# Kernel tuning notes

Hardware: AMD Instinct MI355X
Metric: run time of the kernel (lower is better)

The kernel has to match this reference:

```python
import jax, jax.numpy as jnp
import numpy as np

D = 1024
EXPAND = 2
DI = EXPAND * D
K = 4           # d_conv
C = 64          # chunk_size
ALPHA = 0.9     # memory decay
B, S = 2, 8192
EPS = 1e-5


def setup_inputs() -> dict:
    key = jax.random.key(0)
    ks = jax.random.split(key, 10)
    s = 0.02
    return {
        "x": jax.random.normal(ks[0], (B, S, D), dtype=jnp.float32),
        "norm_w": jnp.ones((D,), dtype=jnp.float32),
        "w_up": jax.random.normal(ks[1], (D, DI), dtype=jnp.float32) * s,
        "w_gate": jax.random.normal(ks[2], (D, DI), dtype=jnp.float32) * s,
        "w_down": jax.random.normal(ks[3], (DI, D), dtype=jnp.float32) * s,
        "conv_w": jax.random.normal(ks[4], (K, 1, DI), dtype=jnp.float32) * s,  # WIO depthwise
        "conv_b": jnp.zeros((DI,), dtype=jnp.float32),
        "wq": jax.random.normal(ks[5], (D, D), dtype=jnp.float32) * s,
        "wk": jax.random.normal(ks[6], (D, D), dtype=jnp.float32) * s,
        "wv": jax.random.normal(ks[7], (D, D), dtype=jnp.float32) * s,
        "wo": jax.random.normal(ks[8], (D, D), dtype=jnp.float32) * s,
    }


def _rmsnorm(x, w):
    ms = jnp.mean(jnp.square(x.astype(jnp.float32)), axis=-1, keepdims=True)
    return (x * jax.lax.rsqrt(ms + EPS).astype(x.dtype)) * w


def _causal_depthwise_conv(u, conv_w, conv_b):
    # u: [B,S,DI]; depthwise causal conv over S, then SiLU
    y = jax.lax.conv_general_dilated(
        u, conv_w,
        window_strides=(1,), padding=[(K - 1, 0)],
        dimension_numbers=("NWC", "WIO", "NWC"),
        feature_group_count=DI)
    return jax.nn.silu(y + conv_b)


def _hebbian_memory(h, wq, wk, wv, wo):
    # chunked linear-attention style Hebbian memory
    b, s, d = h.shape
    n = s // C
    scale = d ** -0.5
    q = (h @ wq).reshape(b, n, C, d) * scale
    k = (h @ wk).reshape(b, n, C, d)
    v = (h @ wv).reshape(b, n, C, d)
    mask = jnp.tril(jnp.ones((C, C), dtype=h.dtype))  # inclusive causal within chunk

    def step(M, qkv):
        qc, kc, vc = qkv  # [b,C,d]
        inter = jnp.einsum("bcd,bde->bce", qc, M)
        attn = jnp.einsum("bcd,bed->bce", qc, kc) * mask
        intra = jnp.einsum("bce,bed->bcd", attn, vc)
        M_new = ALPHA * M + jnp.einsum("bcd,bce->bde", kc, vc)
        return M_new, inter + intra

    M0 = jnp.zeros((b, d, d), dtype=h.dtype)
    qkv = (jnp.swapaxes(q, 0, 1), jnp.swapaxes(k, 0, 1), jnp.swapaxes(v, 0, 1))
    _, o = jax.lax.scan(step, M0, qkv)        # [n,b,C,d]
    o = jnp.swapaxes(o, 0, 1).reshape(b, s, d)
    return o @ wo


def reference(x, norm_w, w_up, w_gate, w_down, conv_w, conv_b, wq, wk, wv, wo):
    normed = _rmsnorm(x, norm_w)
    val = _causal_depthwise_conv(normed @ w_up, conv_w, conv_b)   # [B,S,DI]
    gate = jax.nn.silu(normed @ w_gate)
    out = (gate * val) @ w_down                                   # [B,S,D]
    out = _hebbian_memory(out, wq, wk, wv, wo)
    return x + out
```

## Files before the change

### kernel.cpp

```cpp
#include <hip/hip_runtime.h>
#include <cstdint>
#include <cstddef>

#define SS 8192
#define DD 1024
#define DI2 2048
#define NR 16384

#define LOG2_09 (-0.152003093445050f)
#define LAMBDA16 0.185302018885184f

typedef __attribute__((ext_vector_type(4))) float f32x4;
typedef __attribute__((ext_vector_type(8))) __bf16 bf16x8;

union U16 { uint4 u; bf16x8 b; };

static __device__ __forceinline__ f32x4 MFMA(uint4 a, uint4 b, f32x4 c) {
  U16 ua, ub; ua.u = a; ub.u = b;
  return __builtin_amdgcn_mfma_f32_16x16x32_bf16(ua.b, ub.b, c, 0, 0, 0);
}

static __device__ __forceinline__ unsigned short f2bf(float f) {
  union { float f; unsigned u; } v; v.f = f;
  return (unsigned short)((v.u + 0x7FFFu + ((v.u >> 16) & 1u)) >> 16);
}
static __device__ __forceinline__ float bf2f(unsigned b) {
  union { unsigned u; float f; } v; v.u = b << 16; return v.f;
}
static __device__ __forceinline__ void unpack8(uint4 u, float* f) {
  f[0] = bf2f(u.x & 0xFFFFu); f[1] = bf2f(u.x >> 16);
  f[2] = bf2f(u.y & 0xFFFFu); f[3] = bf2f(u.y >> 16);
  f[4] = bf2f(u.z & 0xFFFFu); f[5] = bf2f(u.z >> 16);
  f[6] = bf2f(u.w & 0xFFFFu); f[7] = bf2f(u.w >> 16);
}

static __device__ __forceinline__ void glds16(const unsigned short* g, char* l) {
  __builtin_amdgcn_global_load_lds(
      (const __attribute__((address_space(1))) unsigned int*)g,
      (__attribute__((address_space(3))) unsigned int*)l, 16, 0, 0);
}

__global__ __launch_bounds__(256)
void transpose_cast(const float* __restrict__ in, unsigned short* __restrict__ out, int R, int Cc) {
  __shared__ float tile[32][33];
  const int r0 = blockIdx.y * 32, c0 = blockIdx.x * 32;
  const int tx = threadIdx.x, ty = threadIdx.y;
#pragma unroll
  for (int i = 0; i < 4; i++)
    tile[ty + i * 8][tx] = in[(size_t)(r0 + ty + i * 8) * Cc + c0 + tx];
  __syncthreads();
#pragma unroll
  for (int i = 0; i < 4; i++)
    out[(size_t)(c0 + ty + i * 8) * R + r0 + tx] = f2bf(tile[tx][ty + i * 8]);
}

__global__ __launch_bounds__(256)
void rmsnorm_kernel(const float* __restrict__ x, const float* __restrict__ w,
                    unsigned short* __restrict__ out) {
  const int row = blockIdx.x, t = threadIdx.x;
  const float4 v = ((const float4*)(x + (size_t)row * DD))[t];
  float ss = v.x * v.x + v.y * v.y + v.z * v.z + v.w * v.w;
  __shared__ float sred[256];
  sred[t] = ss;
  __syncthreads();
  for (int o = 128; o > 0; o >>= 1) {
    if (t < o) sred[t] += sred[t + o];
    __syncthreads();
  }
  const float rr = rsqrtf(sred[0] * (1.0f / (float)DD) + 1e-5f);
  const float4 wv = ((const float4*)w)[t];
  uint2 pk;
  pk.x = (unsigned)f2bf(v.x * rr * wv.x) | ((unsigned)f2bf(v.y * rr * wv.y) << 16);
  pk.y = (unsigned)f2bf(v.z * rr * wv.z) | ((unsigned)f2bf(v.w * rr * wv.w) << 16);
  *(uint2*)(out + (size_t)row * DD + t * 4) = pk;
}

enum { EP_BF16 = 0, EP_BF16_BOTH = 1, EP_BF16_T = 2, EP_F32_RES = 3, EP_STATE = 4,
       EP_SCORE = 6, EP_PVX = 7, EP_QKV = 8 };

template <int MODE>
__global__ __launch_bounds__(512, 2)
void gemm256(const unsigned short* __restrict__ A, const unsigned short* __restrict__ Bt,
             unsigned short* __restrict__ Cb, unsigned short* __restrict__ Ct,
             float* __restrict__ Cf, const float* __restrict__ resid,
             unsigned short* __restrict__ Cx,
             int M, int N, int kLen, int lda, int ldb, float scale) {
  __shared__ char sLds[131072];
  const int t = threadIdx.x, lane = t & 63, wid = t >> 6;
  const int wr = wid >> 2, wc = wid & 3;
  const int l15 = lane & 15, lh = lane >> 4;
  const int mblocks = M >> 8;
  int m0, n0;
  if constexpr (MODE == EP_SCORE) {
    const int p = (int)blockIdx.x;
    const int mt = (p >= 6) ? 3 : (p >= 3) ? 2 : (p >= 1) ? 1 : 0;
    const int nt = p - ((mt * (mt + 1)) >> 1);
    m0 = mt << 8; n0 = nt << 8;
  } else if ((mblocks & 7) == 0) {
    const int msl = mblocks >> 3;
    const int xcd = (int)blockIdx.x & 7, loc = (int)blockIdx.x >> 3;
    m0 = (xcd * msl + (loc % msl)) << 8;
    n0 = (loc / msl) << 8;
  } else {
    m0 = ((int)blockIdx.x % mblocks) << 8;
    n0 = ((int)blockIdx.x / mblocks) << 8;
  }
  int zb = 0, zg = 0;
  const unsigned short* Abase = A;
  const unsigned short* Bbase = Bt;
  if constexpr (MODE == EP_STATE || MODE == EP_SCORE || MODE == EP_PVX) {
    const int gb = blockIdx.z;
    zb = gb >> 3; zg = gb & 7;
    if constexpr (MODE == EP_STATE) {
      Abase = A + (size_t)zb * DD * SS + (size_t)zg * 1024;
      Bbase = Bt + (size_t)zb * DD * SS + (size_t)zg * 1024;
    } else if constexpr (MODE == EP_SCORE) {
      Abase = A + ((size_t)zb * SS + (size_t)zg * 1024) * (size_t)lda;
      Bbase = Bt + ((size_t)zb * SS + (size_t)zg * 1024) * (size_t)ldb;
    } else {
      Abase = A + ((size_t)blockIdx.z << 20);
      Bbase = Bt + (size_t)zb * DD * SS + (size_t)zg * 1024;
    }
  }
  const int srow = wid * 16 + (lane >> 2);
  const int scol = ((lane & 3) << 3) ^ (((srow >> 1) & 3) << 3);
  const unsigned short* pA0 = Abase + (size_t)(m0 + srow) * lda + scol;
  const unsigned short* pA1 = pA0 + (size_t)128 * lda;
  const unsigned short* pB0 = Bbase + (size_t)(n0 + srow) * ldb + scol;
  const unsigned short* pB1 = pB0 + (size_t)128 * ldb;
  const int ldsW = wid * 1024;
  int ntV = 0;
  const unsigned short *pA2 = nullptr, *pA2h = nullptr, *pB2 = nullptr, *pB2h = nullptr;
  if constexpr (MODE == EP_PVX) {
    ntV = ((m0 >> 8) + 1) << 3;
    const unsigned short* qsb = Cx + ((size_t)zb * SS + (size_t)zg * 1024) * DD;
    pA2  = qsb + (size_t)(m0 + srow) * DD + scol;
    pA2h = pA2 + (size_t)128 * DD;
    const unsigned short* mnb = Ct + ((size_t)blockIdx.z << 20);
    pB2  = mnb + (size_t)(n0 + srow) * 1024 + scol;
    pB2h = pB2 + (size_t)128 * 1024;
  }
  int offA[8], offB[4];
#pragma unroll
  for (int mf = 0; mf < 8; mf++) {
    const int r = wr * 128 + mf * 16 + l15;
    offA[mf] = r * 64 + ((lh * 16) ^ (((r >> 1) & 3) << 4));
  }
#pragma unroll
  for (int nf = 0; nf < 4; nf++) {
    const int r = wc * 64 + nf * 16 + l15;
    offB[nf] = r * 64 + ((lh * 16) ^ (((r >> 1) & 3) << 4));
  }
  int NT = kLen >> 5;
  if constexpr (MODE == EP_PVX) NT = ntV + 32;
#define BUFA(tt) (sLds + ((tt) & 3) * 32768)
#define BUFB(tt) (sLds + ((tt) & 3) * 32768 + 16384)
  auto stage = [&](int tt) {
    const int _k = tt * 32;
    const unsigned short* a0 = pA0 + _k;
    const unsigned short* a1 = pA1 + _k;
    const unsigned short* b0 = pB0 + _k;
    const unsigned short* b1 = pB1 + _k;
    if constexpr (MODE == EP_PVX) {
      if (tt >= ntV) {
        const int k2 = (tt - ntV) * 32;
        a0 = pA2 + k2; a1 = pA2h + k2;
        b0 = pB2 + k2; b1 = pB2h + k2;
      }
    }
    glds16(a0, BUFA(tt) + ldsW);
    glds16(a1, BUFA(tt) + 8192 + ldsW);
    glds16(b0, BUFB(tt) + ldsW);
    glds16(b1, BUFB(tt) + 8192 + ldsW);
  };
  stage(0); stage(1); stage(2);
  asm volatile("s_waitcnt vmcnt(8)" ::: "memory");
  __builtin_amdgcn_s_barrier();
  f32x4 acc[8][4] = {};
  for (int kt = 0; kt < NT; ++kt) {
    const char* At  = BUFA(kt);
    const char* Bt_ = BUFB(kt);
    uint4 av[8], bv[4];
#pragma unroll
    for (int i = 0; i < 8; i++) av[i] = *(const uint4*)(At + offA[i]);
#pragma unroll
    for (int i = 0; i < 4; i++) bv[i] = *(const uint4*)(Bt_ + offB[i]);
    if (kt + 3 < NT) stage(kt + 3);
    __builtin_amdgcn_s_setprio(1);
#pragma unroll
    for (int mf = 0; mf < 8; mf++)
#pragma unroll
      for (int nf = 0; nf < 4; nf++)
        acc[mf][nf] = MFMA(av[mf], bv[nf], acc[mf][nf]);
    __builtin_amdgcn_s_setprio(0);
    if (kt < NT - 3)       { asm volatile("s_waitcnt vmcnt(8)" ::: "memory"); }
    else if (kt == NT - 3) { asm volatile("s_waitcnt vmcnt(4)" ::: "memory"); }
    else if (kt == NT - 2) { asm volatile("s_waitcnt vmcnt(0)" ::: "memory"); }
    __builtin_amdgcn_s_barrier();
  }
#undef BUFA
#undef BUFB
#pragma unroll
  for (int mf = 0; mf < 8; mf++) {
    const int r0 = m0 + wr * 128 + mf * 16 + lh * 4;
#pragma unroll
    for (int nf = 0; nf < 4; nf++) {
      const int c = n0 + wc * 64 + nf * 16 + l15;
      f32x4 v = acc[mf][nf] * scale;
      if constexpr (MODE == EP_F32_RES) {
#pragma unroll
        for (int jj = 0; jj < 4; jj++) {
          const size_t idx = (size_t)(r0 + jj) * N + c;
          Cf[idx] = v[jj] + resid[idx];
        }
      } else if constexpr (MODE == EP_STATE) {
        unsigned short* Tg = Cb + ((size_t)blockIdx.z << 20);
#pragma unroll
        for (int jj = 0; jj < 4; jj++)
          Tg[(size_t)(r0 + jj) * 1024 + c] = f2bf(v[jj]);
      } else if constexpr (MODE == EP_SCORE) {
        unsigned short* Sg = Cb + ((size_t)blockIdx.z << 20);
        const int qt = r0 >> 6;
        const int tb = c >> 6;
        float w;
        if (tb > qt)       w = 0.0f;
        else if (tb == qt) w = 1.0f;
        else               w = exp2f((float)(qt - 1 - tb) * LOG2_09);
#pragma unroll
        for (int jj = 0; jj < 4; jj++) {
          float val = v[jj] * w;
          if (tb == qt && (c & 63) > ((r0 + jj) & 63)) val = 0.0f;
          Sg[(size_t)(r0 + jj) * 1024 + c] = f2bf(val);
        }
      } else if constexpr (MODE == EP_PVX) {
#pragma unroll
        for (int jj = 0; jj < 4; jj++)
          Cb[((size_t)zb * SS + (size_t)zg * 1024 + r0 + jj) * DD + c] = f2bf(v[jj]);
      } else if constexpr (MODE == EP_QKV) {
        unsigned short* qb  = Cb;
        unsigned short* kb  = Ct;
        unsigned short* ktb = (unsigned short*)Cf;
        unsigned short* vtb = (unsigned short*)const_cast<float*>(resid);
        const int sect = c >> 10, cc = c & 1023;
        const int bb = r0 >> 13, s0 = r0 & (SS - 1);
        if (sect == 0) {
          const float wq_row = exp2f((float)((s0 >> 6) & 15) * LOG2_09);
#pragma unroll
          for (int jj = 0; jj < 4; jj++) {
            qb[(size_t)(r0 + jj) * DD + cc] = f2bf(v[jj] * 0.03125f);
            Cx[(size_t)(r0 + jj) * DD + cc] = f2bf(v[jj] * 0.03125f * wq_row);
          }
        } else if (sect == 1) {
#pragma unroll
          for (int jj = 0; jj < 4; jj++)
            kb[(size_t)(r0 + jj) * DD + cc] = f2bf(v[jj]);
          const float wt = exp2f((float)(15 - ((s0 >> 6) & 15)) * LOG2_09);
          uint2 pk;
          pk.x = (unsigned)f2bf(v[0] * wt) | ((unsigned)f2bf(v[1] * wt) << 16);
          pk.y = (unsigned)f2bf(v[2] * wt) | ((unsigned)f2bf(v[3] * wt) << 16);
          *(uint2*)(ktb + ((size_t)bb * DD + cc) * SS + s0) = pk;
        } else {
          uint2 pk;
          pk.x = (unsigned)f2bf(v[0]) | ((unsigned)f2bf(v[1]) << 16);
          pk.y = (unsigned)f2bf(v[2]) | ((unsigned)f2bf(v[3]) << 16);
          *(uint2*)(vtb + ((size_t)bb * DD + cc) * SS + s0) = pk;
        }
      } else {
        if constexpr (MODE == EP_BF16 || MODE == EP_BF16_BOTH) {
#pragma unroll
          for (int jj = 0; jj < 4; jj++)
            Cb[(size_t)(r0 + jj) * N + c] = f2bf(v[jj]);
        }
        if constexpr (MODE == EP_BF16_BOTH || MODE == EP_BF16_T) {
          const int bb = r0 >> 13, s0 = r0 & (SS - 1);
          float wt = 1.0f;
          if constexpr (MODE == EP_BF16_BOTH)
            wt = exp2f((float)(15 - ((s0 >> 6) & 15)) * LOG2_09);
          uint2 pk;
          pk.x = (unsigned)f2bf(v[0] * wt) | ((unsigned)f2bf(v[1] * wt) << 16);
          pk.y = (unsigned)f2bf(v[2] * wt) | ((unsigned)f2bf(v[3] * wt) << 16);
          *(uint2*)(Ct + ((size_t)bb * DD + c) * SS + s0) = pk;
        }
      }
    }
  }
}

__global__ __launch_bounds__(256)
void convgate_kernel(const unsigned short* __restrict__ ug, const float* __restrict__ cw,
                     const float* __restrict__ cb, unsigned short* __restrict__ hin) {
  const int r = blockIdx.x;
  const int c0 = threadIdx.x * 8;
  const int s = r & (SS - 1);
  float acc[8];
#pragma unroll
  for (int i = 0; i < 8; i++) acc[i] = cb[c0 + i];
  for (int tap = 0; tap < 4; tap++) {
    const int ds = s - 3 + tap;
    if (ds < 0) continue;
    uint4 uv = *(const uint4*)(ug + (size_t)(r - 3 + tap) * 4096 + c0);
    float u[8]; unpack8(uv, u);
#pragma unroll
    for (int i = 0; i < 8; i++) acc[i] += u[i] * cw[tap * DI2 + c0 + i];
  }
  uint4 gv = *(const uint4*)(ug + (size_t)r * 4096 + DI2 + c0);
  float gt[8]; unpack8(gv, gt);
  unsigned short o16[8];
#pragma unroll
  for (int i = 0; i < 8; i++) {
    const float val = acc[i] / (1.0f + __expf(-acc[i]));
    const float gg  = gt[i] / (1.0f + __expf(-gt[i]));
    o16[i] = f2bf(val * gg);
  }
  uint4 ov;
  ov.x = (unsigned)o16[0] | ((unsigned)o16[1] << 16);
  ov.y = (unsigned)o16[2] | ((unsigned)o16[3] << 16);
  ov.z = (unsigned)o16[4] | ((unsigned)o16[5] << 16);
  ov.w = (unsigned)o16[6] | ((unsigned)o16[7] << 16);
  *(uint4*)(hin + (size_t)r * DI2 + c0) = ov;
}

__global__ __launch_bounds__(256)
void prefix_kernel(unsigned short* __restrict__ Tb) {
  const int tid = blockIdx.x * 256 + threadIdx.x;
  const int b = tid >> 17, i = tid & 131071;
  unsigned short* p = Tb + (((size_t)b * 8) << 20) + (size_t)i * 8;
  float acc[8] = {};
  for (int g = 0; g < 8; g++) {
    unsigned short* pg = p + ((size_t)g << 20);
    uint4 tv = *(uint4*)pg;
    float tf_[8]; unpack8(tv, tf_);
    uint4 ov;
    ov.x = (unsigned)f2bf(acc[0]) | ((unsigned)f2bf(acc[1]) << 16);
    ov.y = (unsigned)f2bf(acc[2]) | ((unsigned)f2bf(acc[3]) << 16);
    ov.z = (unsigned)f2bf(acc[4]) | ((unsigned)f2bf(acc[5]) << 16);
    ov.w = (unsigned)f2bf(acc[6]) | ((unsigned)f2bf(acc[7]) << 16);
    *(uint4*)pg = ov;
#pragma unroll
    for (int e = 0; e < 8; e++) acc[e] = LAMBDA16 * acc[e] + tf_[e];
  }
}

extern "C" void kernel_launch(void* const* d_in, const int* in_sizes, int n_in,
                              void* d_out, int out_size, void* d_ws, size_t ws_size,
                              hipStream_t stream) {
  (void)in_sizes; (void)n_in; (void)out_size;
  const float* x      = (const float*)d_in[0];
  const float* norm_w = (const float*)d_in[1];
  const float* w_up   = (const float*)d_in[2];
  const float* w_gate = (const float*)d_in[3];
  const float* w_down = (const float*)d_in[4];
  const float* conv_w = (const float*)d_in[5];
  const float* conv_b = (const float*)d_in[6];
  const float* wq     = (const float*)d_in[7];
  const float* wk     = (const float*)d_in[8];
  const float* wv     = (const float*)d_in[9];
  const float* wo     = (const float*)d_in[10];
  float* out = (float*)d_out;

  const size_t MB = 1ull << 20;
  if (ws_size < 212 * MB) return;
  char* base = (char*)d_ws;
  unsigned short* ug     = (unsigned short*)(base + 0);
  unsigned short* hbuf   = (unsigned short*)(base + 0);
  unsigned short* Tbuf   = (unsigned short*)(base + 0);
  unsigned short* qbuf   = (unsigned short*)(base + 32 * MB);
  unsigned short* kbuf   = (unsigned short*)(base + 64 * MB);
  unsigned short* obuf   = (unsigned short*)(base + 64 * MB);
  unsigned short* ktbuf  = (unsigned short*)(base + 96 * MB);
  unsigned short* sbuf   = (unsigned short*)(base + 96 * MB);
  unsigned short* normed = (unsigned short*)(base + 128 * MB);
  unsigned short* hin    = (unsigned short*)(base + 128 * MB);
  unsigned short* vtbuf  = (unsigned short*)(base + 128 * MB);
  unsigned short* qsbuf  = (unsigned short*)(base + 160 * MB);
  unsigned short* wugt   = (unsigned short*)(base + 192 * MB);
  unsigned short* wdt    = (unsigned short*)(base + 200 * MB);
  unsigned short* wqkvt  = (unsigned short*)(base + 204 * MB);
  unsigned short* wot    = (unsigned short*)(base + 210 * MB);

  dim3 tb(32, 8);
  transpose_cast<<<dim3(DI2 / 32, DD / 32), tb, 0, stream>>>(w_up,   wugt,                    DD,  DI2);
  transpose_cast<<<dim3(DI2 / 32, DD / 32), tb, 0, stream>>>(w_gate, wugt + (size_t)DI2 * DD, DD,  DI2);
  transpose_cast<<<dim3(DD / 32, DI2 / 32), tb, 0, stream>>>(w_down, wdt, DI2, DD);
  transpose_cast<<<dim3(DD / 32, DD / 32),  tb, 0, stream>>>(wq, wqkvt,                          DD, DD);
  transpose_cast<<<dim3(DD / 32, DD / 32),  tb, 0, stream>>>(wk, wqkvt + (size_t)DD * DD,       DD, DD);
  transpose_cast<<<dim3(DD / 32, DD / 32),  tb, 0, stream>>>(wv, wqkvt + (size_t)2 * DD * DD,   DD, DD);
  transpose_cast<<<dim3(DD / 32, DD / 32),  tb, 0, stream>>>(wo, wot, DD, DD);

  rmsnorm_kernel<<<NR, 256, 0, stream>>>(x, norm_w, normed);

  gemm256<EP_BF16><<<dim3((NR / 256) * (4096 / 256)), 512, 0, stream>>>(
      normed, wugt, ug, nullptr, nullptr, nullptr, nullptr, NR, 4096, DD, DD, DD, 1.0f);

  convgate_kernel<<<NR, 256, 0, stream>>>(ug, conv_w, conv_b, hin);

  gemm256<EP_BF16><<<dim3((NR / 256) * (DD / 256)), 512, 0, stream>>>(
      hin, wdt, hbuf, nullptr, nullptr, nullptr, nullptr, NR, DD, DI2, DI2, DI2, 1.0f);

  gemm256<EP_QKV><<<dim3((NR / 256) * (3072 / 256)), 512, 0, stream>>>(
      hbuf, wqkvt, qbuf, kbuf, (float*)ktbuf, (const float*)vtbuf, qsbuf,
      NR, 3072, DD, DD, DD, 1.0f);

  gemm256<EP_STATE><<<dim3(16, 1, 16), 512, 0, stream>>>(
      vtbuf, ktbuf, Tbuf, nullptr, nullptr, nullptr, nullptr,
      1024, 1024, 1024, SS, SS, 1.0f);
  gemm256<EP_SCORE><<<dim3(10, 1, 16), 512, 0, stream>>>(
      qbuf, kbuf, sbuf, nullptr, nullptr, nullptr, nullptr,
      1024, 1024, 1024, DD, DD, 1.0f);
  prefix_kernel<<<1024, 256, 0, stream>>>(Tbuf);
  gemm256<EP_PVX><<<dim3(16, 1, 16), 512, 0, stream>>>(
      sbuf, vtbuf, obuf, Tbuf, nullptr, nullptr, qsbuf,
      1024, 1024, 1024, 1024, SS, 1.0f);

  gemm256<EP_F32_RES><<<dim3((NR / 256) * (DD / 256)), 512, 0, stream>>>(
      obuf, wot, nullptr, nullptr, out, x, nullptr, NR, DD, DD, DD, DD, 1.0f);
}
```

Measured before the change: 644.3 us.

## Add 8-phase ping-pong GEMM kernel for the dense projection GEMMs

Result: slower. 683.6 us (+6.1%).

```diff
diff --git a/kernel.cpp b/kernel.cpp
--- a/kernel.cpp
+++ b/kernel.cpp
@@ -77,6 +77,200 @@
 
 enum { EP_BF16 = 0, EP_BF16_BOTH = 1, EP_BF16_T = 2, EP_F32_RES = 3, EP_STATE = 4,
        EP_SCORE = 6, EP_PVX = 7, EP_QKV = 8 };
+
+template <int MODE>
+static __device__ __forceinline__ void dense_epilogue(
+    f32x4 (&acc)[8][4], int m0, int n0, int wr, int wc, int l15, int lh,
+    unsigned short* Cb, unsigned short* Ct, float* Cf, const float* resid,
+    unsigned short* Cx, int N, float scale) {
+#pragma unroll
+  for (int mf = 0; mf < 8; mf++) {
+    const int r0 = m0 + wr * 128 + mf * 16 + lh * 4;
+#pragma unroll
+    for (int nf = 0; nf < 4; nf++) {
+      const int c = n0 + wc * 64 + nf * 16 + l15;
+      f32x4 v = acc[mf][nf] * scale;
+      if constexpr (MODE == EP_F32_RES) {
+#pragma unroll
+        for (int jj = 0; jj < 4; jj++) {
+          const size_t idx = (size_t)(r0 + jj) * N + c;
+          Cf[idx] = v[jj] + resid[idx];
+        }
+      } else if constexpr (MODE == EP_QKV) {
+        unsigned short* qb  = Cb;
+        unsigned short* kb  = Ct;
+        unsigned short* ktb = (unsigned short*)Cf;
+        unsigned short* vtb = (unsigned short*)const_cast<float*>(resid);
+        const int sect = c >> 10, cc = c & 1023;
+        const int bb = r0 >> 13, s0 = r0 & (SS - 1);
+        if (sect == 0) {
+          const float wq_row = exp2f((float)((s0 >> 6) & 15) * LOG2_09);
+#pragma unroll
+          for (int jj = 0; jj < 4; jj++) {
+            qb[(size_t)(r0 + jj) * DD + cc] = f2bf(v[jj] * 0.03125f);
+            Cx[(size_t)(r0 + jj) * DD + cc] = f2bf(v[jj] * 0.03125f * wq_row);
+          }
+        } else if (sect == 1) {
+#pragma unroll
+          for (int jj = 0; jj < 4; jj++)
+            kb[(size_t)(r0 + jj) * DD + cc] = f2bf(v[jj]);
+          const float wt = exp2f((float)(15 - ((s0 >> 6) & 15)) * LOG2_09);
+          uint2 pk;
+          pk.x = (unsigned)f2bf(v[0] * wt) | ((unsigned)f2bf(v[1] * wt) << 16);
+          pk.y = (unsigned)f2bf(v[2] * wt) | ((unsigned)f2bf(v[3] * wt) << 16);
+          *(uint2*)(ktb + ((size_t)bb * DD + cc) * SS + s0) = pk;
+        } else {
+          uint2 pk;
+          pk.x = (unsigned)f2bf(v[0]) | ((unsigned)f2bf(v[1]) << 16);
+          pk.y = (unsigned)f2bf(v[2]) | ((unsigned)f2bf(v[3]) << 16);
+          *(uint2*)(vtb + ((size_t)bb * DD + cc) * SS + s0) = pk;
+        }
+      } else {
+#pragma unroll
+        for (int jj = 0; jj < 4; jj++)
+          Cb[(size_t)(r0 + jj) * N + c] = f2bf(v[jj]);
+      }
+    }
+  }
+}
+
+template <int MODE>
+__global__ __launch_bounds__(512, 2)
+void gemm8p(const unsigned short* __restrict__ A, const unsigned short* __restrict__ Bt,
+            unsigned short* __restrict__ Cb, unsigned short* __restrict__ Ct,
+            float* __restrict__ Cf, const float* __restrict__ resid,
+            unsigned short* __restrict__ Cx,
+            int M, int N, int kLen, int lda, int ldb, float scale) {
+  __shared__ char sLds[131072];
+  const int t = threadIdx.x, lane = t & 63, wid = t >> 6;
+  const int wr = wid >> 2, wc = wid & 3;
+  const int l15 = lane & 15, lh = lane >> 4;
+  const int mblocks = M >> 8;
+  int m0, n0;
+  if ((mblocks & 7) == 0) {
+    const int msl = mblocks >> 3;
+    const int xcd = (int)blockIdx.x & 7, loc = (int)blockIdx.x >> 3;
+    m0 = (xcd * msl + (loc % msl)) << 8;
+    n0 = (loc / msl) << 8;
+  } else {
+    m0 = ((int)blockIdx.x % mblocks) << 8;
+    n0 = ((int)blockIdx.x / mblocks) << 8;
+  }
+  const int rA = wid * 16 + (lane >> 3);
+  const int scol = (((lane & 7) ^ ((lane >> 3) & 7))) * 8;
+  const int NT = kLen >> 6;
+  int offA[2][8], offB[2][4];
+#pragma unroll
+  for (int qm = 0; qm < 2; qm++)
+#pragma unroll
+    for (int mfl = 0; mfl < 4; mfl++)
+#pragma unroll
+      for (int kk = 0; kk < 2; kk++) {
+        const int Rl = qm * 64 + mfl * 16 + l15;
+        offA[qm][mfl * 2 + kk] = wr * 16384 + Rl * 128 +
+                                 ((kk * 64 + lh * 16) ^ ((Rl & 7) << 4));
+      }
+#pragma unroll
+  for (int qn = 0; qn < 2; qn++)
+#pragma unroll
+    for (int nfl = 0; nfl < 2; nfl++)
+#pragma unroll
+      for (int kk = 0; kk < 2; kk++) {
+        const int Rl = (wc & 1) * 64 + (qn * 2 + nfl) * 16 + l15;
+        offB[qn][nfl * 2 + kk] = 65536 + (wc >> 1) * 16384 + Rl * 128 +
+                                 ((kk * 64 + lh * 16) ^ ((Rl & 7) << 4));
+      }
+  auto stageA = [&](int tile, int h) {
+    const unsigned short* src = A + (size_t)(m0 + h * 128 + rA) * lda + (size_t)tile * 64 + scol;
+    char* slot = sLds + (((tile & 1) * 2 + h) * 16384) + wid * 2048;
+    glds16(src, slot);
+    glds16(src + (size_t)8 * lda, slot + 1024);
+  };
+  auto stageB = [&](int tile, int h) {
+    const unsigned short* src = Bt + (size_t)(n0 + h * 128 + rA) * ldb + (size_t)tile * 64 + scol;
+    char* slot = sLds + 65536 + (((tile & 1) * 2 + h) * 16384) + wid * 2048;
+    glds16(src, slot);
+    glds16(src + (size_t)8 * ldb, slot + 1024);
+  };
+  stageB(0, 0); stageB(0, 1); stageA(0, 0); stageA(0, 1);
+  if (NT > 1) { stageB(1, 0); stageB(1, 1); }
+  asm volatile("s_waitcnt vmcnt(4)" ::: "memory");
+  __builtin_amdgcn_s_barrier();
+  f32x4 acc[8][4] = {};
+  uint4 av0[8], av1[8], bv0[4], bv1[4];
+  for (int kt = 0; kt < NT; ++kt) {
+    const int pb = (kt & 1) * 32768;
+    const char* L = sLds + pb;
+#pragma unroll
+    for (int i = 0; i < 8; i++) av0[i] = *(const uint4*)(L + offA[0][i]);
+#pragma unroll
+    for (int i = 0; i < 4; i++) bv0[i] = *(const uint4*)(L + offB[0][i]);
+    if (kt + 1 < NT) stageA(kt + 1, 0);
+    __builtin_amdgcn_s_barrier();
+    asm volatile("s_waitcnt lgkmcnt(0)" ::: "memory");
+    __builtin_amdgcn_sched_barrier(0);
+    __builtin_amdgcn_s_setprio(1);
+#pragma unroll
+    for (int mf = 0; mf < 4; mf++)
+#pragma unroll
+      for (int nf = 0; nf < 2; nf++)
+#pragma unroll
+        for (int kk = 0; kk < 2; kk++)
+          acc[mf][nf] = MFMA(av0[mf * 2 + kk], bv0[nf * 2 + kk], acc[mf][nf]);
+    __builtin_amdgcn_s_setprio(0);
+    __builtin_amdgcn_s_barrier();
+#pragma unroll
+    for (int i = 0; i < 4; i++) bv1[i] = *(const uint4*)(L + offB[1][i]);
+    if (kt + 1 < NT) stageA(kt + 1, 1);
+    __builtin_amdgcn_s_barrier();
+    asm volatile("s_waitcnt lgkmcnt(0)" ::: "memory");
+    __builtin_amdgcn_sched_barrier(0);
+    __builtin_amdgcn_s_setprio(1);
+#pragma unroll
+    for (int mf = 0; mf < 4; mf++)
+#pragma unroll
+      for (int nf = 0; nf < 2; nf++)
+#pragma unroll
+        for (int kk = 0; kk < 2; kk++)
+          acc[mf][2 + nf] = MFMA(av0[mf * 2 + kk], bv1[nf * 2 + kk], acc[mf][2 + nf]);
+    __builtin_amdgcn_s_setprio(0);
+    __builtin_amdgcn_s_barrier();
+#pragma unroll
+    for (int i = 0; i < 8; i++) av1[i] = *(const uint4*)(L + offA[1][i]);
+    if (kt + 2 < NT) stageB(kt + 2, 0);
+    __builtin_amdgcn_s_barrier();
+    asm volatile("s_waitcnt lgkmcnt(0)" ::: "memory");
+    __builtin_amdgcn_sched_barrier(0);
+    __builtin_amdgcn_s_setprio(1);
+#pragma unroll
+    for (int mf = 0; mf < 4; mf++)
+#pragma unroll
+      for (int nf = 0; nf < 2; nf++)
+#pragma unroll
+        for (int kk = 0; kk < 2; kk++)
+          acc[4 + mf][2 + nf] = MFMA(av1[mf * 2 + kk], bv1[nf * 2 + kk], acc[4 + mf][2 + nf]);
+    __builtin_amdgcn_s_setprio(0);
+    __builtin_amdgcn_s_barrier();
+    if (kt + 2 < NT) {
+      stageB(kt + 2, 1);
+      asm volatile("s_waitcnt vmcnt(4)" ::: "memory");
+    } else if (kt + 1 < NT) {
+      asm volatile("s_waitcnt vmcnt(0)" ::: "memory");
+    }
+    __builtin_amdgcn_s_barrier();
+    __builtin_amdgcn_s_setprio(1);
+#pragma unroll
+    for (int mf = 0; mf < 4; mf++)
+#pragma unroll
+      for (int nf = 0; nf < 2; nf++)
+#pragma unroll
+        for (int kk = 0; kk < 2; kk++)
+          acc[4 + mf][nf] = MFMA(av1[mf * 2 + kk], bv0[nf * 2 + kk], acc[4 + mf][nf]);
+    __builtin_amdgcn_s_setprio(0);
+    __builtin_amdgcn_s_barrier();
+  }
+  dense_epilogue<MODE>(acc, m0, n0, wr, wc, l15, lh, Cb, Ct, Cf, resid, Cx, N, scale);
+}
 
 template <int MODE>
 __global__ __launch_bounds__(512, 2)
@@ -96,11 +290,6 @@
     const int mt = (p >= 6) ? 3 : (p >= 3) ? 2 : (p >= 1) ? 1 : 0;
     const int nt = p - ((mt * (mt + 1)) >> 1);
     m0 = mt << 8; n0 = nt << 8;
-  } else if ((mblocks & 7) == 0) {
-    const int msl = mblocks >> 3;
-    const int xcd = (int)blockIdx.x & 7, loc = (int)blockIdx.x >> 3;
-    m0 = (xcd * msl + (loc % msl)) << 8;
-    n0 = (loc / msl) << 8;
   } else {
     m0 = ((int)blockIdx.x % mblocks) << 8;
     n0 = ((int)blockIdx.x / mblocks) << 8;
@@ -108,7 +297,7 @@
   int zb = 0, zg = 0;
   const unsigned short* Abase = A;
   const unsigned short* Bbase = Bt;
-  if constexpr (MODE == EP_STATE || MODE == EP_SCORE || MODE == EP_PVX) {
+  {
     const int gb = blockIdx.z;
     zb = gb >> 3; zg = gb & 7;
     if constexpr (MODE == EP_STATE) {
@@ -207,13 +396,7 @@
     for (int nf = 0; nf < 4; nf++) {
       const int c = n0 + wc * 64 + nf * 16 + l15;
       f32x4 v = acc[mf][nf] * scale;
-      if constexpr (MODE == EP_F32_RES) {
-#pragma unroll
-        for (int jj = 0; jj < 4; jj++) {
-          const size_t idx = (size_t)(r0 + jj) * N + c;
-          Cf[idx] = v[jj] + resid[idx];
-        }
-      } else if constexpr (MODE == EP_STATE) {
+      if constexpr (MODE == EP_STATE) {
         unsigned short* Tg = Cb + ((size_t)blockIdx.z << 20);
 #pragma unroll
         for (int jj = 0; jj < 4; jj++)
@@ -236,51 +419,6 @@
 #pragma unroll
         for (int jj = 0; jj < 4; jj++)
           Cb[((size_t)zb * SS + (size_t)zg * 1024 + r0 + jj) * DD + c] = f2bf(v[jj]);
-      } else if constexpr (MODE == EP_QKV) {
-        unsigned short* qb  = Cb;
-        unsigned short* kb  = Ct;
-        unsigned short* ktb = (unsigned short*)Cf;
-        unsigned short* vtb = (unsigned short*)const_cast<float*>(resid);
-        const int sect = c >> 10, cc = c & 1023;
-        const int bb = r0 >> 13, s0 = r0 & (SS - 1);
-        if (sect == 0) {
-          const float wq_row = exp2f((float)((s0 >> 6) & 15) * LOG2_09);
-#pragma unroll
-          for (int jj = 0; jj < 4; jj++) {
-            qb[(size_t)(r0 + jj) * DD + cc] = f2bf(v[jj] * 0.03125f);
-            Cx[(size_t)(r0 + jj) * DD + cc] = f2bf(v[jj] * 0.03125f * wq_row);
-          }
-        } else if (sect == 1) {
-#pragma unroll
-          for (int jj = 0; jj < 4; jj++)
-            kb[(size_t)(r0 + jj) * DD + cc] = f2bf(v[jj]);
-          const float wt = exp2f((float)(15 - ((s0 >> 6) & 15)) * LOG2_09);
-          uint2 pk;
-          pk.x = (unsigned)f2bf(v[0] * wt) | ((unsigned)f2bf(v[1] * wt) << 16);
-          pk.y = (unsigned)f2bf(v[2] * wt) | ((unsigned)f2bf(v[3] * wt) << 16);
-          *(uint2*)(ktb + ((size_t)bb * DD + cc) * SS + s0) = pk;
-        } else {
-          uint2 pk;
-          pk.x = (unsigned)f2bf(v[0]) | ((unsigned)f2bf(v[1]) << 16);
-          pk.y = (unsigned)f2bf(v[2]) | ((unsigned)f2bf(v[3]) << 16);
-          *(uint2*)(vtb + ((size_t)bb * DD + cc) * SS + s0) = pk;
-        }
-      } else {
-        if constexpr (MODE == EP_BF16 || MODE == EP_BF16_BOTH) {
-#pragma unroll
-          for (int jj = 0; jj < 4; jj++)
-            Cb[(size_t)(r0 + jj) * N + c] = f2bf(v[jj]);
-        }
-        if constexpr (MODE == EP_BF16_BOTH || MODE == EP_BF16_T) {
-          const int bb = r0 >> 13, s0 = r0 & (SS - 1);
-          float wt = 1.0f;
-          if constexpr (MODE == EP_BF16_BOTH)
-            wt = exp2f((float)(15 - ((s0 >> 6) & 15)) * LOG2_09);
-          uint2 pk;
-          pk.x = (unsigned)f2bf(v[0] * wt) | ((unsigned)f2bf(v[1] * wt) << 16);
-          pk.y = (unsigned)f2bf(v[2] * wt) | ((unsigned)f2bf(v[3] * wt) << 16);
-          *(uint2*)(Ct + ((size_t)bb * DD + c) * SS + s0) = pk;
-        }
       }
     }
   }
@@ -389,15 +527,15 @@
 
   rmsnorm_kernel<<<NR, 256, 0, stream>>>(x, norm_w, normed);
 
-  gemm256<EP_BF16><<<dim3((NR / 256) * (4096 / 256)), 512, 0, stream>>>(
+  gemm8p<EP_BF16><<<dim3((NR / 256) * (4096 / 256)), 512, 0, stream>>>(
       normed, wugt, ug, nullptr, nullptr, nullptr, nullptr, NR, 4096, DD, DD, DD, 1.0f);
 
   convgate_kernel<<<NR, 256, 0, stream>>>(ug, conv_w, conv_b, hin);
 
-  gemm256<EP_BF16><<<dim3((NR / 256) * (DD / 256)), 512, 0, stream>>>(
+  gemm8p<EP_BF16><<<dim3((NR / 256) * (DD / 256)), 512, 0, stream>>>(
       hin, wdt, hbuf, nullptr, nullptr, nullptr, nullptr, NR, DD, DI2, DI2, DI2, 1.0f);
 
-  gemm256<EP_QKV><<<dim3((NR / 256) * (3072 / 256)), 512, 0, stream>>>(
+  gemm8p<EP_QKV><<<dim3((NR / 256) * (3072 / 256)), 512, 0, stream>>>(
       hbuf, wqkvt, qbuf, kbuf, (float*)ktbuf, (const float*)vtbuf, qsbuf,
       NR, 3072, DD, DD, DD, 1.0f);
 
@@ -412,6 +550,6 @@
       sbuf, vtbuf, obuf, Tbuf, nullptr, nullptr, qsbuf,
       1024, 1024, 1024, 1024, SS, 1.0f);
 
-  gemm256<EP_F32_RES><<<dim3((NR / 256) * (DD / 256)), 512, 0, stream>>>(
+  gemm8p<EP_F32_RES><<<dim3((NR / 256) * (DD / 256)), 512, 0, stream>>>(
       obuf, wot, nullptr, nullptr, out, x, nullptr, NR, DD, DD, DD, DD, 1.0f);
 }
```

## Fuse state and score GEMMs into one launch and drop duplicate scaled-q buffer

Applied to the files above, without the earlier changes.

Result: no change. 648.3 us (+0.6%).

```diff
diff --git a/kernel.cpp b/kernel.cpp
--- a/kernel.cpp
+++ b/kernel.cpp
@@ -75,8 +75,7 @@
   *(uint2*)(out + (size_t)row * DD + t * 4) = pk;
 }
 
-enum { EP_BF16 = 0, EP_BF16_BOTH = 1, EP_BF16_T = 2, EP_F32_RES = 3, EP_STATE = 4,
-       EP_SCORE = 6, EP_PVX = 7, EP_QKV = 8 };
+enum { EP_BF16 = 0, EP_F32_RES = 3, EP_PVX = 7, EP_QKV = 8 };
 
 template <int MODE>
 __global__ __launch_bounds__(512, 2)
@@ -91,12 +90,7 @@
   const int l15 = lane & 15, lh = lane >> 4;
   const int mblocks = M >> 8;
   int m0, n0;
-  if constexpr (MODE == EP_SCORE) {
-    const int p = (int)blockIdx.x;
-    const int mt = (p >= 6) ? 3 : (p >= 3) ? 2 : (p >= 1) ? 1 : 0;
-    const int nt = p - ((mt * (mt + 1)) >> 1);
-    m0 = mt << 8; n0 = nt << 8;
-  } else if ((mblocks & 7) == 0) {
+  if ((mblocks & 7) == 0) {
     const int msl = mblocks >> 3;
     const int xcd = (int)blockIdx.x & 7, loc = (int)blockIdx.x >> 3;
     m0 = (xcd * msl + (loc % msl)) << 8;
@@ -108,19 +102,11 @@
   int zb = 0, zg = 0;
   const unsigned short* Abase = A;
   const unsigned short* Bbase = Bt;
-  if constexpr (MODE == EP_STATE || MODE == EP_SCORE || MODE == EP_PVX) {
+  if constexpr (MODE == EP_PVX) {
     const int gb = blockIdx.z;
     zb = gb >> 3; zg = gb & 7;
-    if constexpr (MODE == EP_STATE) {
-      Abase = A + (size_t)zb * DD * SS + (size_t)zg * 1024;
-      Bbase = Bt + (size_t)zb * DD * SS + (size_t)zg * 1024;
-    } else if constexpr (MODE == EP_SCORE) {
-      Abase = A + ((size_t)zb * SS + (size_t)zg * 1024) * (size_t)lda;
-      Bbase = Bt + ((size_t)zb * SS + (size_t)zg * 1024) * (size_t)ldb;
-    } else {
-      Abase = A + ((size_t)blockIdx.z << 20);
-      Bbase = Bt + (size_t)zb * DD * SS + (size_t)zg * 1024;
-    }
+    Abase = A + ((size_t)blockIdx.z << 20);
+    Bbase = Bt + (size_t)zb * DD * SS + (size_t)zg * 1024;
   }
   const int srow = wid * 16 + (lane >> 2);
   const int scol = ((lane & 3) << 3) ^ (((srow >> 1) & 3) << 3);
@@ -213,25 +199,6 @@
           const size_t idx = (size_t)(r0 + jj) * N + c;
           Cf[idx] = v[jj] + resid[idx];
         }
-      } else if constexpr (MODE == EP_STATE) {
-        unsigned short* Tg = Cb + ((size_t)blockIdx.z << 20);
-#pragma unroll
-        for (int jj = 0; jj < 4; jj++)
-          Tg[(size_t)(r0 + jj) * 1024 + c] = f2bf(v[jj]);
-      } else if constexpr (MODE == EP_SCORE) {
-        unsigned short* Sg = Cb + ((size_t)blockIdx.z << 20);
-        const int qt = r0 >> 6;
-        const int tb = c >> 6;
-        float w;
-        if (tb > qt)       w = 0.0f;
-        else if (tb == qt) w = 1.0f;
-        else               w = exp2f((float)(qt - 1 - tb) * LOG2_09);
-#pragma unroll
-        for (int jj = 0; jj < 4; jj++) {
-          float val = v[jj] * w;
-          if (tb == qt && (c & 63) > ((r0 + jj) & 63)) val = 0.0f;
-          Sg[(size_t)(r0 + jj) * 1024 + c] = f2bf(val);
-        }
       } else if constexpr (MODE == EP_PVX) {
 #pragma unroll
         for (int jj = 0; jj < 4; jj++)
@@ -246,10 +213,8 @@
         if (sect == 0) {
           const float wq_row = exp2f((float)((s0 >> 6) & 15) * LOG2_09);
 #pragma unroll
-          for (int jj = 0; jj < 4; jj++) {
-            qb[(size_t)(r0 + jj) * DD + cc] = f2bf(v[jj] * 0.03125f);
-            Cx[(size_t)(r0 + jj) * DD + cc] = f2bf(v[jj] * 0.03125f * wq_row);
-          }
+          for (int jj = 0; jj < 4; jj++)
+            qb[(size_t)(r0 + jj) * DD + cc] = f2bf(v[jj] * 0.03125f * wq_row);
         } else if (sect == 1) {
 #pragma unroll
           for (int jj = 0; jj < 4; jj++)
@@ -266,20 +231,120 @@
           *(uint2*)(vtb + ((size_t)bb * DD + cc) * SS + s0) = pk;
         }
       } else {
-        if constexpr (MODE == EP_BF16 || MODE == EP_BF16_BOTH) {
-#pragma unroll
-          for (int jj = 0; jj < 4; jj++)
-            Cb[(size_t)(r0 + jj) * N + c] = f2bf(v[jj]);
-        }
-        if constexpr (MODE == EP_BF16_BOTH || MODE == EP_BF16_T) {
-          const int bb = r0 >> 13, s0 = r0 & (SS - 1);
-          float wt = 1.0f;
-          if constexpr (MODE == EP_BF16_BOTH)
-            wt = exp2f((float)(15 - ((s0 >> 6) & 15)) * LOG2_09);
-          uint2 pk;
-          pk.x = (unsigned)f2bf(v[0] * wt) | ((unsigned)f2bf(v[1] * wt) << 16);
-          pk.y = (unsigned)f2bf(v[2] * wt) | ((unsigned)f2bf(v[3] * wt) << 16);
-          *(uint2*)(Ct + ((size_t)bb * DD + c) * SS + s0) = pk;
+#pragma unroll
+        for (int jj = 0; jj < 4; jj++)
+          Cb[(size_t)(r0 + jj) * N + c] = f2bf(v[jj]);
+      }
+    }
+  }
+}
+
+__global__ __launch_bounds__(512, 2)
+void hebb_sg(const unsigned short* __restrict__ vt, const unsigned short* __restrict__ kt,
+             const unsigned short* __restrict__ q, const unsigned short* __restrict__ k,
+             unsigned short* __restrict__ Tb, unsigned short* __restrict__ Sb) {
+  __shared__ char sLds[131072];
+  const int t = threadIdx.x, lane = t & 63, wid = t >> 6;
+  const int wr = wid >> 2, wc = wid & 3;
+  const int l15 = lane & 15, lh = lane >> 4;
+  const int zb = (int)blockIdx.z >> 3, zg = (int)blockIdx.z & 7;
+  const bool isScore = (int)blockIdx.x >= 16;
+  int m0, n0, ld;
+  const unsigned short *Abase, *Bbase;
+  if (!isScore) {
+    const int x = (int)blockIdx.x;
+    m0 = (x & 3) << 8; n0 = (x >> 2) << 8;
+    Abase = vt + (size_t)zb * DD * SS + (size_t)zg * 1024;
+    Bbase = kt + (size_t)zb * DD * SS + (size_t)zg * 1024;
+    ld = SS;
+  } else {
+    const int p = (int)blockIdx.x - 16;
+    const int mt = (p >= 6) ? 3 : (p >= 3) ? 2 : (p >= 1) ? 1 : 0;
+    const int nt = p - ((mt * (mt + 1)) >> 1);
+    m0 = mt << 8; n0 = nt << 8;
+    Abase = q + ((size_t)zb * SS + (size_t)zg * 1024) * DD;
+    Bbase = k + ((size_t)zb * SS + (size_t)zg * 1024) * DD;
+    ld = DD;
+  }
+  const int srow = wid * 16 + (lane >> 2);
+  const int scol = ((lane & 3) << 3) ^ (((srow >> 1) & 3) << 3);
+  const unsigned short* pA0 = Abase + (size_t)(m0 + srow) * ld + scol;
+  const unsigned short* pA1 = pA0 + (size_t)128 * ld;
+  const unsigned short* pB0 = Bbase + (size_t)(n0 + srow) * ld + scol;
+  const unsigned short* pB1 = pB0 + (size_t)128 * ld;
+  const int ldsW = wid * 1024;
+  int offA[8], offB[4];
+#pragma unroll
+  for (int mf = 0; mf < 8; mf++) {
+    const int r = wr * 128 + mf * 16 + l15;
+    offA[mf] = r * 64 + ((lh * 16) ^ (((r >> 1) & 3) << 4));
+  }
+#pragma unroll
+  for (int nf = 0; nf < 4; nf++) {
+    const int r = wc * 64 + nf * 16 + l15;
+    offB[nf] = r * 64 + ((lh * 16) ^ (((r >> 1) & 3) << 4));
+  }
+  const int NT = 32;
+#define BUFA(tt) (sLds + ((tt) & 3) * 32768)
+#define BUFB(tt) (sLds + ((tt) & 3) * 32768 + 16384)
+  auto stage = [&](int tt) {
+    const int _k = tt * 32;
+    glds16(pA0 + _k, BUFA(tt) + ldsW);
+    glds16(pA1 + _k, BUFA(tt) + 8192 + ldsW);
+    glds16(pB0 + _k, BUFB(tt) + ldsW);
+    glds16(pB1 + _k, BUFB(tt) + 8192 + ldsW);
+  };
+  stage(0); stage(1); stage(2);
+  asm volatile("s_waitcnt vmcnt(8)" ::: "memory");
+  __builtin_amdgcn_s_barrier();
+  f32x4 acc[8][4] = {};
+  for (int kt2 = 0; kt2 < NT; ++kt2) {
+    const char* At  = BUFA(kt2);
+    const char* Bt_ = BUFB(kt2);
+    uint4 av[8], bv[4];
+#pragma unroll
+    for (int i = 0; i < 8; i++) av[i] = *(const uint4*)(At + offA[i]);
+#pragma unroll
+    for (int i = 0; i < 4; i++) bv[i] = *(const uint4*)(Bt_ + offB[i]);
+    if (kt2 + 3 < NT) stage(kt2 + 3);
+    __builtin_amdgcn_s_setprio(1);
+#pragma unroll
+    for (int mf = 0; mf < 8; mf++)
+#pragma unroll
+      for (int nf = 0; nf < 4; nf++)
+        acc[mf][nf] = MFMA(av[mf], bv[nf], acc[mf][nf]);
+    __builtin_amdgcn_s_setprio(0);
+    if (kt2 < NT - 3)       { asm volatile("s_waitcnt vmcnt(8)" ::: "memory"); }
+    else if (kt2 == NT - 3) { asm volatile("s_waitcnt vmcnt(4)" ::: "memory"); }
+    else if (kt2 == NT - 2) { asm volatile("s_waitcnt vmcnt(0)" ::: "memory"); }
+    __builtin_amdgcn_s_barrier();
+  }
+#undef BUFA
+#undef BUFB
+#pragma unroll
+  for (int mf = 0; mf < 8; mf++) {
+    const int r0 = m0 + wr * 128 + mf * 16 + lh * 4;
+#pragma unroll
+    for (int nf = 0; nf < 4; nf++) {
+      const int c = n0 + wc * 64 + nf * 16 + l15;
+      if (!isScore) {
+        unsigned short* Tg = Tb + ((size_t)blockIdx.z << 20);
+#pragma unroll
+        for (int jj = 0; jj < 4; jj++)
+          Tg[(size_t)(r0 + jj) * 1024 + c] = f2bf(acc[mf][nf][jj]);
+      } else {
+        unsigned short* Sg = Sb + ((size_t)blockIdx.z << 20);
+        const int qt = r0 >> 6;
+        const int tb = c >> 6;
+        float w;
+        if (tb > qt)       w = 0.0f;
+        else if (tb == qt) w = exp2f((float)(-qt) * LOG2_09);
+        else               w = exp2f((float)(-1 - tb) * LOG2_09);
+#pragma unroll
+        for (int jj = 0; jj < 4; jj++) {
+          float val = acc[mf][nf][jj] * w;
+          if (tb == qt && (c & 63) > ((r0 + jj) & 63)) val = 0.0f;
+          Sg[(size_t)(r0 + jj) * 1024 + c] = f2bf(val);
         }
       }
     }
@@ -368,11 +433,10 @@
   unsigned short* kbuf   = (unsigned short*)(base + 64 * MB);
   unsigned short* obuf   = (unsigned short*)(base + 64 * MB);
   unsigned short* ktbuf  = (unsigned short*)(base + 96 * MB);
-  unsigned short* sbuf   = (unsigned short*)(base + 96 * MB);
   unsigned short* normed = (unsigned short*)(base + 128 * MB);
   unsigned short* hin    = (unsigned short*)(base + 128 * MB);
   unsigned short* vtbuf  = (unsigned short*)(base + 128 * MB);
-  unsigned short* qsbuf  = (unsigned short*)(base + 160 * MB);
+  unsigned short* sbuf   = (unsigned short*)(base + 160 * MB);
   unsigned short* wugt   = (unsigned short*)(base + 192 * MB);
   unsigned short* wdt    = (unsigned short*)(base + 200 * MB);
   unsigned short* wqkvt  = (unsigned short*)(base + 204 * MB);
@@ -398,18 +462,13 @@
       hin, wdt, hbuf, nullptr, nullptr, nullptr, nullptr, NR, DD, DI2, DI2, DI2, 1.0f);
 
   gemm256<EP_QKV><<<dim3((NR / 256) * (3072 / 256)), 512, 0, stream>>>(
-      hbuf, wqkvt, qbuf, kbuf, (float*)ktbuf, (const float*)vtbuf, qsbuf,
+      hbuf, wqkvt, qbuf, kbuf, (float*)ktbuf, (const float*)vtbuf, nullptr,
       NR, 3072, DD, DD, DD, 1.0f);
 
-  gemm256<EP_STATE><<<dim3(16, 1, 16), 512, 0, stream>>>(
-      vtbuf, ktbuf, Tbuf, nullptr, nullptr, nullptr, nullptr,
-      1024, 1024, 1024, SS, SS, 1.0f);
-  gemm256<EP_SCORE><<<dim3(10, 1, 16), 512, 0, stream>>>(
-      qbuf, kbuf, sbuf, nullptr, nullptr, nullptr, nullptr,
-      1024, 1024, 1024, DD, DD, 1.0f);
+  hebb_sg<<<dim3(26, 1, 16), 512, 0, stream>>>(vtbuf, ktbuf, qbuf, kbuf, Tbuf, sbuf);
   prefix_kernel<<<1024, 256, 0, stream>>>(Tbuf);
   gemm256<EP_PVX><<<dim3(16, 1, 16), 512, 0, stream>>>(
-      sbuf, vtbuf, obuf, Tbuf, nullptr, nullptr, qsbuf,
+      sbuf, vtbuf, obuf, Tbuf, nullptr, nullptr, qbuf,
       1024, 1024, 1024, 1024, SS, 1.0f);
 
   gemm256<EP_F32_RES><<<dim3((NR / 256) * (DD / 256)), 512, 0, stream>>>(
```

## Switch GEMM to 64-wide K tiles with double buffering and 8-row swizzle

Applied to the files above, without the earlier changes.

Measured after the change: 693.7 us. +7.7%, slower.

```diff
diff --git a/kernel.cpp b/kernel.cpp
--- a/kernel.cpp
+++ b/kernel.cpp
@@ -75,8 +75,7 @@
   *(uint2*)(out + (size_t)row * DD + t * 4) = pk;
 }
 
-enum { EP_BF16 = 0, EP_BF16_BOTH = 1, EP_BF16_T = 2, EP_F32_RES = 3, EP_STATE = 4,
-       EP_SCORE = 6, EP_PVX = 7, EP_QKV = 8 };
+enum { EP_BF16 = 0, EP_F32_RES = 3, EP_STATE = 4, EP_SCORE = 6, EP_PVX = 7, EP_QKV = 8 };
 
 template <int MODE>
 __global__ __launch_bounds__(512, 2)
@@ -122,80 +121,78 @@
       Bbase = Bt + (size_t)zb * DD * SS + (size_t)zg * 1024;
     }
   }
-  const int srow = wid * 16 + (lane >> 2);
-  const int scol = ((lane & 3) << 3) ^ (((srow >> 1) & 3) << 3);
-  const unsigned short* pA0 = Abase + (size_t)(m0 + srow) * lda + scol;
-  const unsigned short* pA1 = pA0 + (size_t)128 * lda;
-  const unsigned short* pB0 = Bbase + (size_t)(n0 + srow) * ldb + scol;
-  const unsigned short* pB1 = pB0 + (size_t)128 * ldb;
-  const int ldsW = wid * 1024;
+  const int rr8 = wid * 8 + (lane >> 3);
+  const int sc8 = (((lane & 7) ^ ((lane >> 3) & 7))) * 8;
+  const unsigned short* pAr = Abase + (size_t)(m0 + rr8) * lda + sc8;
+  const unsigned short* pBr = Bbase + (size_t)(n0 + rr8) * ldb + sc8;
   int ntV = 0;
-  const unsigned short *pA2 = nullptr, *pA2h = nullptr, *pB2 = nullptr, *pB2h = nullptr;
+  const unsigned short *pA2r = nullptr, *pB2r = nullptr;
   if constexpr (MODE == EP_PVX) {
-    ntV = ((m0 >> 8) + 1) << 3;
+    ntV = ((m0 >> 8) + 1) << 2;
     const unsigned short* qsb = Cx + ((size_t)zb * SS + (size_t)zg * 1024) * DD;
-    pA2  = qsb + (size_t)(m0 + srow) * DD + scol;
-    pA2h = pA2 + (size_t)128 * DD;
+    pA2r = qsb + (size_t)(m0 + rr8) * DD + sc8;
     const unsigned short* mnb = Ct + ((size_t)blockIdx.z << 20);
-    pB2  = mnb + (size_t)(n0 + srow) * 1024 + scol;
-    pB2h = pB2 + (size_t)128 * 1024;
-  }
-  int offA[8], offB[4];
+    pB2r = mnb + (size_t)(n0 + rr8) * 1024 + sc8;
+  }
+  int offA[8][2], offB[4][2];
 #pragma unroll
   for (int mf = 0; mf < 8; mf++) {
     const int r = wr * 128 + mf * 16 + l15;
-    offA[mf] = r * 64 + ((lh * 16) ^ (((r >> 1) & 3) << 4));
+#pragma unroll
+    for (int kk = 0; kk < 2; kk++)
+      offA[mf][kk] = r * 128 + ((kk * 64 + lh * 16) ^ ((r & 7) << 4));
   }
 #pragma unroll
   for (int nf = 0; nf < 4; nf++) {
     const int r = wc * 64 + nf * 16 + l15;
-    offB[nf] = r * 64 + ((lh * 16) ^ (((r >> 1) & 3) << 4));
-  }
-  int NT = kLen >> 5;
-  if constexpr (MODE == EP_PVX) NT = ntV + 32;
-#define BUFA(tt) (sLds + ((tt) & 3) * 32768)
-#define BUFB(tt) (sLds + ((tt) & 3) * 32768 + 16384)
+#pragma unroll
+    for (int kk = 0; kk < 2; kk++)
+      offB[nf][kk] = r * 128 + ((kk * 64 + lh * 16) ^ ((r & 7) << 4));
+  }
+  int NT = kLen >> 6;
+  if constexpr (MODE == EP_PVX) NT = ntV + 16;
+#define BUFA(tt) (sLds + ((tt) & 1) * 65536)
+#define BUFB(tt) (sLds + ((tt) & 1) * 65536 + 32768)
   auto stage = [&](int tt) {
-    const int _k = tt * 32;
-    const unsigned short* a0 = pA0 + _k;
-    const unsigned short* a1 = pA1 + _k;
-    const unsigned short* b0 = pB0 + _k;
-    const unsigned short* b1 = pB1 + _k;
+    const unsigned short* a = pAr;
+    const unsigned short* b = pBr;
+    size_t la = lda, lb = ldb;
+    int ke = tt * 64;
     if constexpr (MODE == EP_PVX) {
-      if (tt >= ntV) {
-        const int k2 = (tt - ntV) * 32;
-        a0 = pA2 + k2; a1 = pA2h + k2;
-        b0 = pB2 + k2; b1 = pB2h + k2;
-      }
+      if (tt >= ntV) { a = pA2r; b = pB2r; la = DD; lb = 1024; ke = (tt - ntV) * 64; }
     }
-    glds16(a0, BUFA(tt) + ldsW);
-    glds16(a1, BUFA(tt) + 8192 + ldsW);
-    glds16(b0, BUFB(tt) + ldsW);
-    glds16(b1, BUFB(tt) + 8192 + ldsW);
+    char* BA = BUFA(tt) + wid * 1024;
+    char* BB = BUFB(tt) + wid * 1024;
+#pragma unroll
+    for (int h = 0; h < 4; h++) {
+      glds16(a + (size_t)(h * 64) * la + ke, BA + h * 8192);
+      glds16(b + (size_t)(h * 64) * lb + ke, BB + h * 8192);
+    }
   };
-  stage(0); stage(1); stage(2);
-  asm volatile("s_waitcnt vmcnt(8)" ::: "memory");
+  stage(0);
+  asm volatile("s_waitcnt vmcnt(0)" ::: "memory");
   __builtin_amdgcn_s_barrier();
   f32x4 acc[8][4] = {};
   for (int kt = 0; kt < NT; ++kt) {
     const char* At  = BUFA(kt);
     const char* Bt_ = BUFB(kt);
-    uint4 av[8], bv[4];
-#pragma unroll
-    for (int i = 0; i < 8; i++) av[i] = *(const uint4*)(At + offA[i]);
-#pragma unroll
-    for (int i = 0; i < 4; i++) bv[i] = *(const uint4*)(Bt_ + offB[i]);
-    if (kt + 3 < NT) stage(kt + 3);
-    __builtin_amdgcn_s_setprio(1);
-#pragma unroll
-    for (int mf = 0; mf < 8; mf++)
-#pragma unroll
-      for (int nf = 0; nf < 4; nf++)
-        acc[mf][nf] = MFMA(av[mf], bv[nf], acc[mf][nf]);
-    __builtin_amdgcn_s_setprio(0);
-    if (kt < NT - 3)       { asm volatile("s_waitcnt vmcnt(8)" ::: "memory"); }
-    else if (kt == NT - 3) { asm volatile("s_waitcnt vmcnt(4)" ::: "memory"); }
-    else if (kt == NT - 2) { asm volatile("s_waitcnt vmcnt(0)" ::: "memory"); }
+    if (kt + 1 < NT) stage(kt + 1);
+#pragma unroll
+    for (int kk = 0; kk < 2; kk++) {
+      uint4 av[8], bv[4];
+#pragma unroll
+      for (int i = 0; i < 8; i++) av[i] = *(const uint4*)(At + offA[i][kk]);
+#pragma unroll
+      for (int i = 0; i < 4; i++) bv[i] = *(const uint4*)(Bt_ + offB[i][kk]);
+      __builtin_amdgcn_s_setprio(1);
+#pragma unroll
+      for (int mf = 0; mf < 8; mf++)
+#pragma unroll
+        for (int nf = 0; nf < 4; nf++)
+          acc[mf][nf] = MFMA(av[mf], bv[nf], acc[mf][nf]);
+      __builtin_amdgcn_s_setprio(0);
+    }
+    asm volatile("s_waitcnt vmcnt(0)" ::: "memory");
     __builtin_amdgcn_s_barrier();
   }
 #undef BUFA
@@ -266,21 +263,9 @@
           *(uint2*)(vtb + ((size_t)bb * DD + cc) * SS + s0) = pk;
         }
       } else {
-        if constexpr (MODE == EP_BF16 || MODE == EP_BF16_BOTH) {
-#pragma unroll
-          for (int jj = 0; jj < 4; jj++)
-            Cb[(size_t)(r0 + jj) * N + c] = f2bf(v[jj]);
-        }
-        if constexpr (MODE == EP_BF16_BOTH || MODE == EP_BF16_T) {
-          const int bb = r0 >> 13, s0 = r0 & (SS - 1);
-          float wt = 1.0f;
-          if constexpr (MODE == EP_BF16_BOTH)
-            wt = exp2f((float)(15 - ((s0 >> 6) & 15)) * LOG2_09);
-          uint2 pk;
-          pk.x = (unsigned)f2bf(v[0] * wt) | ((unsigned)f2bf(v[1] * wt) << 16);
-          pk.y = (unsigned)f2bf(v[2] * wt) | ((unsigned)f2bf(v[3] * wt) << 16);
-          *(uint2*)(Ct + ((size_t)bb * DD + c) * SS + s0) = pk;
-        }
+#pragma unroll
+        for (int jj = 0; jj < 4; jj++)
+          Cb[(size_t)(r0 + jj) * N + c] = f2bf(v[jj]);
       }
     }
   }
```
